# Performance work log

Measured on AMD Instinct MI355X. Metric: run time of the kernel, lower is better.

## Reference

```python
import jax, jax.numpy as jnp
import numpy as np

LOG_2PI = float(np.log(2.0 * np.pi))


def setup_inputs() -> dict:
    key = jax.random.key(0)
    k1, k2 = jax.random.split(key)
    M, N, D = 8192, 16384, 16
    x_eval = jax.random.normal(k1, (M, D), dtype=jnp.float32)
    x_base = jax.random.normal(k2, (N, D), dtype=jnp.float32)
    # module stores log_bw = log(bw_init); use log(0.2)
    log_bw = jnp.full((1,), np.log(0.2), dtype=jnp.float32)
    return {"x_eval": x_eval, "x_base": x_base, "log_bw": log_bw}


def reference(x_eval, x_base, log_bw):
    N = x_base.shape[0]
    D = x_base.shape[1]
    bw2 = jnp.exp(2.0 * log_bw)  # bw ** 2, shape [1]
    # pairwise squared distances [M, N] via the gemm-based expansion
    sq_e = jnp.sum(x_eval * x_eval, axis=1, keepdims=True)          # [M, 1]
    sq_b = jnp.sum(x_base * x_base, axis=1, keepdims=True).T        # [1, N]
    cross = jnp.einsum('md,nd->mn', x_eval, x_base)                 # [M, N]
    d2 = sq_e + sq_b - 2.0 * cross                                  # [M, N]
    t2 = -0.5 * d2 / bw2                                            # log Gaussian kernel
    t1 = -0.5 * D * LOG_2PI - log_bw                                # scalar-ish [1]
    val = jnp.exp(t1 + t2).sum(axis=1) / N                          # [M]
    return val
```

## Files before the change

### kernel.cpp

```cpp
#include <hip/hip_runtime.h>
#include <math.h>


#define LOG_2PI_F 1.8378770664093453f
#define LOG2E_F   1.4426950408889634f
#define TH_SKIP   -110.0f

#define M_PTS 8192
#define N_PTS 16384
#define NCH   64
#define ROWS_PER_CHUNK (N_PTS / NCH)
#define TPC (ROWS_PER_CHUNK / 32)
#define TILE_USH 1536
#define CHUNK_USH (TPC * TILE_USH)

typedef __attribute__((ext_vector_type(8)))  short bf16x8;
typedef __attribute__((ext_vector_type(16))) float f32x16;

static __device__ __forceinline__ unsigned short f2bf(float x) {
    unsigned u = __float_as_uint(x);
    u += 0x7fffu + ((u >> 16) & 1u);
    return (unsigned short)(u >> 16);
}
static __device__ __forceinline__ float bf2f(unsigned short h) {
    return __uint_as_float(((unsigned)h) << 16);
}
static __device__ __forceinline__ uint4 pack8(const unsigned short* a) {
    uint4 u;
    u.x = (unsigned)a[0] | ((unsigned)a[1] << 16);
    u.y = (unsigned)a[2] | ((unsigned)a[3] << 16);
    u.z = (unsigned)a[4] | ((unsigned)a[5] << 16);
    u.w = (unsigned)a[6] | ((unsigned)a[7] << 16);
    return u;
}

__global__ __launch_bounds__(256) void kde_pack10(
        const float* __restrict__ xe, const float* __restrict__ xb,
        const float* __restrict__ log_bw,
        unsigned short* __restrict__ bint,
        unsigned short* __restrict__ eh, unsigned short* __restrict__ el,
        unsigned short* __restrict__ en) {
    int r = blockIdx.x * 256 + threadIdx.x;
    if (r >= N_PTS + M_PTS) return;
    const float k2l = __expf(-2.f * log_bw[0]) * LOG2E_F;

    int is_eval = (r >= N_PTS);
    int rr = is_eval ? (r - N_PTS) : r;
    const float* src = is_eval ? xe : xb;
    float dscale = is_eval ? k2l : 1.0f;

    const float4* row = (const float4*)(src + (size_t)rr * 16);
    unsigned short hs[16], ls[16], ns[16];
    float s = 0.f;
#pragma unroll
    for (int k = 0; k < 4; ++k) {
        float4 v = row[k];
        float c[4] = {v.x, v.y, v.z, v.w};
#pragma unroll
        for (int j = 0; j < 4; ++j) {
            s = fmaf(c[j], c[j], s);
            float d = c[j] * dscale;
            unsigned short h = f2bf(d);
            hs[k*4+j] = h;
            ls[k*4+j] = f2bf(d - bf2f(h));
        }
    }
    float cn = -0.5f * s * k2l;
    unsigned short c0 = f2bf(cn);
    float r1 = cn - bf2f(c0);
    unsigned short c1 = f2bf(r1);
    unsigned short c2 = f2bf(r1 - bf2f(c1));
#pragma unroll
    for (int i = 0; i < 16; ++i) ns[i] = 0;
    if (is_eval) {
        ns[0] = 0x3F80; ns[1] = 0x3F80; ns[2] = 0x3F80;
        ns[3] = c0;     ns[4] = c1;     ns[5] = c2;
    } else {
        ns[0] = c0;     ns[1] = c1;     ns[2] = c2;
        ns[3] = 0x3F80; ns[4] = 0x3F80; ns[5] = 0x3F80;
    }

    if (is_eval) {
        uint4* dh = (uint4*)(eh + (size_t)rr * 16);
        uint4* dl = (uint4*)(el + (size_t)rr * 16);
        uint4* dn = (uint4*)(en + (size_t)rr * 16);
        dh[0] = pack8(hs); dh[1] = pack8(hs + 8);
        dl[0] = pack8(ls); dl[1] = pack8(ls + 8);
        dn[0] = pack8(ns); dn[1] = pack8(ns + 8);
    } else {
        int t = rr >> 5, q = rr & 31;
        unsigned short* base = bint + (size_t)t * TILE_USH + q * 16;
        uint4* dh = (uint4*)(base);
        uint4* dl = (uint4*)(base + 512);
        uint4* dn = (uint4*)(base + 1024);
        dh[0] = pack8(hs); dh[1] = pack8(hs + 8);
        dl[0] = pack8(ls); dl[1] = pack8(ls + 8);
        dn[0] = pack8(ns); dn[1] = pack8(ns + 8);
    }
}

__global__ __launch_bounds__(256, 8) void kde_main10(
        const unsigned short* __restrict__ eh, const unsigned short* __restrict__ el,
        const unsigned short* __restrict__ en,
        const unsigned short* __restrict__ bint,
        float* __restrict__ part) {
    const int lane = threadIdx.x & 63;
    const int widx = threadIdx.x >> 6;
    const int b = blockIdx.x;
    const int chunk = b >> 6;
    const int etp = (b & 63) * 4 + widx;
    const int col = lane & 31;
    const int kg  = lane >> 5;

    const size_t eoff = ((size_t)etp * 32 + col) * 16 + (size_t)kg * 8;
    const bf16x8 Bh = *(const bf16x8*)(eh + eoff);
    const bf16x8 Bl = *(const bf16x8*)(el + eoff);
    const bf16x8 Bn = *(const bf16x8*)(en + eoff);

    const unsigned short* pa =
        bint + (size_t)chunk * CHUNK_USH + (size_t)col * 16 + (size_t)kg * 8;

    float acc0 = 0.f, acc1 = 0.f;

#pragma unroll 1
    for (int t = 0; t < TPC; ++t) {
        const bf16x8 Ah = *(const bf16x8*)(pa);
        const bf16x8 Al = *(const bf16x8*)(pa + 512);
        const bf16x8 An = *(const bf16x8*)(pa + 1024);
        pa += TILE_USH;

        f32x16 C;
#pragma unroll
        for (int r = 0; r < 16; ++r) C[r] = 0.f;
        C = __builtin_amdgcn_mfma_f32_32x32x16_bf16(Ah, Bh, C, 0, 0, 0);
        C = __builtin_amdgcn_mfma_f32_32x32x16_bf16(Ah, Bl, C, 0, 0, 0);
        C = __builtin_amdgcn_mfma_f32_32x32x16_bf16(Al, Bh, C, 0, 0, 0);
        C = __builtin_amdgcn_mfma_f32_32x32x16_bf16(An, Bn, C, 0, 0, 0);

#pragma unroll
        for (int r = 0; r < 16; r += 4) {
            float g = fmaxf(fmaxf(C[r], C[r+1]), fmaxf(C[r+2], C[r+3]));
            if (__any(g > TH_SKIP)) {
                acc0 += __builtin_amdgcn_exp2f(C[r]);
                acc1 += __builtin_amdgcn_exp2f(C[r+1]);
                acc0 += __builtin_amdgcn_exp2f(C[r+2]);
                acc1 += __builtin_amdgcn_exp2f(C[r+3]);
            }
        }
    }

    float s = acc0 + acc1;
    s += __shfl_xor(s, 32, 64);
    if (lane < 32)
        part[(size_t)chunk * M_PTS + (size_t)etp * 32 + col] = s;
}

__global__ __launch_bounds__(256) void kde_red10(
        const float* __restrict__ part, const float* __restrict__ log_bw,
        float* __restrict__ out) {
    int m = blockIdx.x * 256 + threadIdx.x;
    if (m >= M_PTS) return;
    float lb = log_bw[0];
    float scale = __expf(-8.f * LOG_2PI_F - lb) / (float)N_PTS;
    float s = 0.f;
#pragma unroll
    for (int c = 0; c < NCH; ++c) s += part[(size_t)c * M_PTS + m];
    out[m] = scale * s;
}

extern "C" void kernel_launch(void* const* d_in, const int* in_sizes, int n_in,
                              void* d_out, int out_size, void* d_ws, size_t ws_size,
                              hipStream_t stream) {
    const float* xe = (const float*)d_in[0];
    const float* xb = (const float*)d_in[1];
    const float* lb = (const float*)d_in[2];
    float* out = (float*)d_out;

    unsigned short* bint = (unsigned short*)d_ws;
    unsigned short* eh = bint + (size_t)(N_PTS / 32) * TILE_USH;
    unsigned short* el = eh + (size_t)M_PTS * 16;
    unsigned short* en = el + (size_t)M_PTS * 16;
    float* part = (float*)(en + (size_t)M_PTS * 16);

    kde_pack10<<<(N_PTS + M_PTS) / 256, 256, 0, stream>>>(xe, xb, lb,
                                                          bint, eh, el, en);
    kde_main10<<<4096, 256, 0, stream>>>(eh, el, en, bint, part);
    kde_red10<<<M_PTS / 256, 256, 0, stream>>>(part, lb, out);
}
```

Before: 47.87 us.

## Fuse bf16 split packing into main MFMA kernel using shared-memory tiles

Drops the separate pack kernel. Each block now converts its 256 base rows into hi/lo/norm bf16 tiles in shared memory, and each wave converts its own eval rows to MFMA operands in registers, using a lane shuffle to complete the squared norm. This removes one kernel launch and the workspace round trip for the packed operands. In exchange, the packing work is recomputed redundantly across the 64 blocks that share each chunk, and a block-wide barrier plus LDS traffic is added.

```diff
diff --git a/kernel.cpp b/kernel.cpp
--- a/kernel.cpp
+++ b/kernel.cpp
@@ -11,8 +11,6 @@
 #define NCH   64
 #define ROWS_PER_CHUNK (N_PTS / NCH)
 #define TPC (ROWS_PER_CHUNK / 32)
-#define TILE_USH 1536
-#define CHUNK_USH (TPC * TILE_USH)
 
 typedef __attribute__((ext_vector_type(8)))  short bf16x8;
 typedef __attribute__((ext_vector_type(16))) float f32x16;
@@ -34,100 +32,101 @@
     return u;
 }
 
-__global__ __launch_bounds__(256) void kde_pack10(
+__global__ __launch_bounds__(256) void kde_fused12(
         const float* __restrict__ xe, const float* __restrict__ xb,
-        const float* __restrict__ log_bw,
-        unsigned short* __restrict__ bint,
-        unsigned short* __restrict__ eh, unsigned short* __restrict__ el,
-        unsigned short* __restrict__ en) {
-    int r = blockIdx.x * 256 + threadIdx.x;
-    if (r >= N_PTS + M_PTS) return;
-    const float k2l = __expf(-2.f * log_bw[0]) * LOG2E_F;
+        const float* __restrict__ log_bw, float* __restrict__ part) {
+    __shared__ unsigned short As[TPC][3][32][16];
 
-    int is_eval = (r >= N_PTS);
-    int rr = is_eval ? (r - N_PTS) : r;
-    const float* src = is_eval ? xe : xb;
-    float dscale = is_eval ? k2l : 1.0f;
-
-    const float4* row = (const float4*)(src + (size_t)rr * 16);
-    unsigned short hs[16], ls[16], ns[16];
-    float s = 0.f;
-#pragma unroll
-    for (int k = 0; k < 4; ++k) {
-        float4 v = row[k];
-        float c[4] = {v.x, v.y, v.z, v.w};
-#pragma unroll
-        for (int j = 0; j < 4; ++j) {
-            s = fmaf(c[j], c[j], s);
-            float d = c[j] * dscale;
-            unsigned short h = f2bf(d);
-            hs[k*4+j] = h;
-            ls[k*4+j] = f2bf(d - bf2f(h));
-        }
-    }
-    float cn = -0.5f * s * k2l;
-    unsigned short c0 = f2bf(cn);
-    float r1 = cn - bf2f(c0);
-    unsigned short c1 = f2bf(r1);
-    unsigned short c2 = f2bf(r1 - bf2f(c1));
-#pragma unroll
-    for (int i = 0; i < 16; ++i) ns[i] = 0;
-    if (is_eval) {
-        ns[0] = 0x3F80; ns[1] = 0x3F80; ns[2] = 0x3F80;
-        ns[3] = c0;     ns[4] = c1;     ns[5] = c2;
-    } else {
-        ns[0] = c0;     ns[1] = c1;     ns[2] = c2;
-        ns[3] = 0x3F80; ns[4] = 0x3F80; ns[5] = 0x3F80;
-    }
-
-    if (is_eval) {
-        uint4* dh = (uint4*)(eh + (size_t)rr * 16);
-        uint4* dl = (uint4*)(el + (size_t)rr * 16);
-        uint4* dn = (uint4*)(en + (size_t)rr * 16);
-        dh[0] = pack8(hs); dh[1] = pack8(hs + 8);
-        dl[0] = pack8(ls); dl[1] = pack8(ls + 8);
-        dn[0] = pack8(ns); dn[1] = pack8(ns + 8);
-    } else {
-        int t = rr >> 5, q = rr & 31;
-        unsigned short* base = bint + (size_t)t * TILE_USH + q * 16;
-        uint4* dh = (uint4*)(base);
-        uint4* dl = (uint4*)(base + 512);
-        uint4* dn = (uint4*)(base + 1024);
-        dh[0] = pack8(hs); dh[1] = pack8(hs + 8);
-        dl[0] = pack8(ls); dl[1] = pack8(ls + 8);
-        dn[0] = pack8(ns); dn[1] = pack8(ns + 8);
-    }
-}
-
-__global__ __launch_bounds__(256, 8) void kde_main10(
-        const unsigned short* __restrict__ eh, const unsigned short* __restrict__ el,
-        const unsigned short* __restrict__ en,
-        const unsigned short* __restrict__ bint,
-        float* __restrict__ part) {
-    const int lane = threadIdx.x & 63;
-    const int widx = threadIdx.x >> 6;
+    const int tid  = threadIdx.x;
+    const int lane = tid & 63;
+    const int widx = tid >> 6;
     const int b = blockIdx.x;
     const int chunk = b >> 6;
     const int etp = (b & 63) * 4 + widx;
     const int col = lane & 31;
     const int kg  = lane >> 5;
 
-    const size_t eoff = ((size_t)etp * 32 + col) * 16 + (size_t)kg * 8;
-    const bf16x8 Bh = *(const bf16x8*)(eh + eoff);
-    const bf16x8 Bl = *(const bf16x8*)(el + eoff);
-    const bf16x8 Bn = *(const bf16x8*)(en + eoff);
+    const float k2l = __expf(-2.f * log_bw[0]) * LOG2E_F;
 
-    const unsigned short* pa =
-        bint + (size_t)chunk * CHUNK_USH + (size_t)col * 16 + (size_t)kg * 8;
+    {
+        const int t = tid >> 5, q = tid & 31;
+        const float4* row = (const float4*)(xb + ((size_t)chunk * ROWS_PER_CHUNK + tid) * 16);
+        unsigned short hs[16], ls[16], ns[16];
+        float s = 0.f;
+#pragma unroll
+        for (int k = 0; k < 4; ++k) {
+            float4 v = row[k];
+            float c[4] = {v.x, v.y, v.z, v.w};
+#pragma unroll
+            for (int j = 0; j < 4; ++j) {
+                s = fmaf(c[j], c[j], s);
+                unsigned short h = f2bf(c[j]);
+                hs[k*4+j] = h;
+                ls[k*4+j] = f2bf(c[j] - bf2f(h));
+            }
+        }
+        float cn = -0.5f * s * k2l;
+        unsigned short c0 = f2bf(cn);
+        float r1 = cn - bf2f(c0);
+        unsigned short c1 = f2bf(r1);
+        unsigned short c2 = f2bf(r1 - bf2f(c1));
+#pragma unroll
+        for (int i = 0; i < 16; ++i) ns[i] = 0;
+        ns[0] = c0; ns[1] = c1; ns[2] = c2;
+        ns[3] = 0x3F80; ns[4] = 0x3F80; ns[5] = 0x3F80;
+
+        uint4* dh = (uint4*)&As[t][0][q][0];
+        dh[0] = pack8(hs); dh[1] = pack8(hs + 8);
+        uint4* dl = (uint4*)&As[t][1][q][0];
+        dl[0] = pack8(ls); dl[1] = pack8(ls + 8);
+        uint4* dn = (uint4*)&As[t][2][q][0];
+        dn[0] = pack8(ns); dn[1] = pack8(ns + 8);
+    }
+
+    bf16x8 Bh, Bl, Bn;
+    {
+        const float4* erow =
+            (const float4*)(xe + ((size_t)(etp * 32 + col)) * 16 + (size_t)kg * 8);
+        float4 v0 = erow[0], v1 = erow[1];
+        float c[8] = {v0.x, v0.y, v0.z, v0.w, v1.x, v1.y, v1.z, v1.w};
+        unsigned short hs[8], ls[8];
+        float s = 0.f;
+#pragma unroll
+        for (int j = 0; j < 8; ++j) {
+            s = fmaf(c[j], c[j], s);
+            float d = c[j] * k2l;
+            unsigned short h = f2bf(d);
+            hs[j] = h;
+            ls[j] = f2bf(d - bf2f(h));
+        }
+        s += __shfl_xor(s, 32, 64);
+        float cn = -0.5f * s * k2l;
+        unsigned short c0 = f2bf(cn);
+        float r1 = cn - bf2f(c0);
+        unsigned short c1 = f2bf(r1);
+        unsigned short c2 = f2bf(r1 - bf2f(c1));
+
+        uint4 uh = pack8(hs), ul = pack8(ls);
+        Bh = *(const bf16x8*)&uh;
+        Bl = *(const bf16x8*)&ul;
+        unsigned short nsv[8] = {0,0,0,0,0,0,0,0};
+        if (kg == 0) {
+            nsv[0] = 0x3F80; nsv[1] = 0x3F80; nsv[2] = 0x3F80;
+            nsv[3] = c0;     nsv[4] = c1;     nsv[5] = c2;
+        }
+        uint4 un = pack8(nsv);
+        Bn = *(const bf16x8*)&un;
+    }
+
+    __syncthreads();
 
     float acc0 = 0.f, acc1 = 0.f;
 
 #pragma unroll 1
     for (int t = 0; t < TPC; ++t) {
-        const bf16x8 Ah = *(const bf16x8*)(pa);
-        const bf16x8 Al = *(const bf16x8*)(pa + 512);
-        const bf16x8 An = *(const bf16x8*)(pa + 1024);
-        pa += TILE_USH;
+        const bf16x8 Ah = *(const bf16x8*)&As[t][0][col][kg * 8];
+        const bf16x8 Al = *(const bf16x8*)&As[t][1][col][kg * 8];
+        const bf16x8 An = *(const bf16x8*)&As[t][2][col][kg * 8];
 
         f32x16 C;
 #pragma unroll
@@ -155,7 +154,7 @@
         part[(size_t)chunk * M_PTS + (size_t)etp * 32 + col] = s;
 }
 
-__global__ __launch_bounds__(256) void kde_red10(
+__global__ __launch_bounds__(256) void kde_red12(
         const float* __restrict__ part, const float* __restrict__ log_bw,
         float* __restrict__ out) {
     int m = blockIdx.x * 256 + threadIdx.x;
@@ -176,14 +175,8 @@
     const float* lb = (const float*)d_in[2];
     float* out = (float*)d_out;
 
-    unsigned short* bint = (unsigned short*)d_ws;
-    unsigned short* eh = bint + (size_t)(N_PTS / 32) * TILE_USH;
-    unsigned short* el = eh + (size_t)M_PTS * 16;
-    unsigned short* en = el + (size_t)M_PTS * 16;
-    float* part = (float*)(en + (size_t)M_PTS * 16);
+    float* part = (float*)d_ws;
 
-    kde_pack10<<<(N_PTS + M_PTS) / 256, 256, 0, stream>>>(xe, xb, lb,
-                                                          bint, eh, el, en);
-    kde_main10<<<4096, 256, 0, stream>>>(eh, el, en, bint, part);
-    kde_red10<<<M_PTS / 256, 256, 0, stream>>>(part, lb, out);
+    kde_fused12<<<4096, 256, 0, stream>>>(xe, xb, lb, part);
+    kde_red12<<<M_PTS / 256, 256, 0, stream>>>(part, lb, out);
 }
```

After: 46.12 us. -3.6%, faster.
